# Kernel optimization log

Measured on AMD Instinct MI355X. Metric: run time of the kernel, lower is better.

The kernel has to match this reference:

```python
import jax, jax.numpy as jnp
import numpy as np

B = 4          # documents per batch
L = 128        # unique candidate entity links
S = 2048       # predicted spans (max over batch)
N = 1 + L + S  # root + links + spans


def setup_inputs() -> dict:
    key = jax.random.key(0)
    k1, k2, k3 = jax.random.split(key, 3)
    # coref/linking edge scores over [root | links | spans] x [root | links | spans]
    scores = jax.random.normal(k1, (B, N, N), dtype=jnp.float32) * 0.1
    eye = jnp.eye(N, dtype=jnp.float32)
    # z mask: all admissible edges -- no self loops, no incoming edges to root
    z_mask = jnp.ones((B, N, N), dtype=jnp.float32) * (1.0 - eye)[None]
    z_mask = z_mask.at[:, :, 0].set(0.0)
    # target mask: sparse subset of z edges + root->all so a spanning
    # arborescence always exists (mirrors the gold cluster / gold link edges)
    tgt = (jax.random.uniform(k2, (B, N, N)) < 0.05).astype(jnp.float32) * z_mask
    tgt = tgt.at[:, 0, 1:].set(1.0)
    # ragged valid lengths per batch element (1 + unique_links_len + n_pred_spans)
    lengths = jnp.array([N, N - 256, N - 512, N - 64], dtype=jnp.int32)
    return {"scores": scores, "target_mask": tgt, "z_mask": z_mask, "lengths": lengths}


def _mtt_log_partition(scores, mask, lengths):
    """Matrix-tree theorem log-partition: logdet of the root-minor of the
    Laplacian of exp(scores) restricted to edges in `mask` and to the first
    `lengths[b]` nodes of each batch element."""
    n = scores.shape[-1]
    valid = (jnp.arange(n)[None, :] < lengths[:, None]).astype(scores.dtype)  # [B,N]
    w = jnp.exp(scores) * mask * valid[:, :, None] * valid[:, None, :]        # [B,N,N]
    colsum = jnp.sum(w, axis=-2)                                              # incoming weight per node
    lap = colsum[:, :, None] * jnp.eye(n, dtype=scores.dtype)[None] - w       # L = D_in - W
    minor = lap[:, 1:, 1:]                                                    # drop root row/col
    # pad the diagonal of invalid (past-length) nodes with 1 so they
    # contribute logdet 0 instead of making the minor singular
    pad = 1.0 - valid[:, 1:]
    minor = minor + pad[:, :, None] * jnp.eye(n - 1, dtype=scores.dtype)[None]
    _, logdet = jnp.linalg.slogdet(minor)
    return logdet


def reference(scores, target_mask, z_mask, lengths):
    log_z = _mtt_log_partition(scores, z_mask, lengths)        # log partition over all arborescences
    log_t = _mtt_log_partition(scores, target_mask, lengths)   # log weight of gold arborescences
    return jnp.mean(log_z - log_t)                             # MTT negative log-likelihood
```

## Files before the change

### kernel.cpp

```cpp
#include <hip/hip_runtime.h>
#include <math.h>

#define NFULL 2177
#define NN    2176
#define NB    64
#define NMAT  8
#define NBATCH 4


__global__ void init_cs_kernel(float* __restrict__ cs) {
  int i = blockIdx.x * blockDim.x + threadIdx.x;
  if (i < NMAT * NN) cs[i] = 0.f;
}

__global__ void colsum_kernel(const float* __restrict__ scores,
                              const float* __restrict__ zm,
                              const float* __restrict__ tm,
                              const int* __restrict__ lengths,
                              float* __restrict__ cs) {
  int c = blockIdx.x * blockDim.x + threadIdx.x;
  if (c >= NN) return;
  int rc = blockIdx.y;
  int b  = blockIdx.z;
  int len = lengths[b];
  int j = c + 1;
  if (j >= len) return;
  int i0 = rc * 128;
  int i1 = i0 + 128; if (i1 > len) i1 = len;
  if (i0 >= i1) return;
  size_t base = (size_t)b * NFULL * NFULL + j;
  float az = 0.f, at = 0.f;
  for (int i = i0; i < i1; ++i) {
    size_t off = base + (size_t)i * NFULL;
    float e = __expf(scores[off]);
    az += e * zm[off];
    at += e * tm[off];
  }
  atomicAdd(&cs[b * NN + c], az);
  atomicAdd(&cs[(NBATCH + b) * NN + c], at);
}

__global__ void build_kernel(const float* __restrict__ scores,
                             const float* __restrict__ zm,
                             const float* __restrict__ tm,
                             const int* __restrict__ lengths,
                             const float* __restrict__ cs,
                             float* __restrict__ M) {
  int c = blockIdx.x * blockDim.x + threadIdx.x;
  if (c >= NN) return;
  int r = blockIdx.y;
  int b = blockIdx.z;
  int len = lengths[b];
  int i = r + 1, j = c + 1;
  float vz = 0.f, vt = 0.f;
  if (i < len && j < len) {
    size_t off = (size_t)b * NFULL * NFULL + (size_t)i * NFULL + j;
    float e = __expf(scores[off]);
    vz = e * zm[off];
    vt = e * tm[off];
  }
  float dz = 0.f, dt = 0.f;
  if (r == c) {
    float pad = (j < len) ? 0.f : 1.f;
    dz = cs[b * NN + c] + pad;
    dt = cs[(NBATCH + b) * NN + c] + pad;
  }
  size_t mo = (size_t)r * NN + c;
  M[(size_t)b * NN * NN + mo]            = dz - vz;
  M[(size_t)(NBATCH + b) * NN * NN + mo] = dt - vt;
}


__global__ __launch_bounds__(256) void factor_diag(float* __restrict__ Mb, int k0) {
  __shared__ float T[64][65];
  int m = blockIdx.x;
  float* A = Mb + (size_t)m * NN * NN;
  int tid = threadIdx.x;
  for (int idx = tid; idx < 64 * 64; idx += 256) {
    int r = idx >> 6, c = idx & 63;
    T[r][c] = A[(size_t)(k0 + r) * NN + (k0 + c)];
  }
  __syncthreads();
  for (int j = 0; j < 63; ++j) {
    float inv = 1.0f / T[j][j];
    for (int r = j + 1 + tid; r < 64; r += 256) T[r][j] *= inv;
    __syncthreads();
    int rem = 63 - j;
    for (int idx = tid; idx < rem * rem; idx += 256) {
      int rr = j + 1 + idx / rem;
      int cc = j + 1 + idx % rem;
      T[rr][cc] -= T[rr][j] * T[j][cc];
    }
    __syncthreads();
  }
  for (int idx = tid; idx < 64 * 64; idx += 256) {
    int r = idx >> 6, c = idx & 63;
    A[(size_t)(k0 + r) * NN + (k0 + c)] = T[r][c];
  }
}

__global__ __launch_bounds__(64) void panel_solve(float* __restrict__ Mb, int k0) {
  __shared__ float D[64][65];
  __shared__ float T[64][65];
  int m    = blockIdx.y;
  int role = blockIdx.z;
  float* A = Mb + (size_t)m * NN * NN;
  int tid = threadIdx.x;
  int obase = k0 + 64 + blockIdx.x * 64;
  for (int idx = tid; idx < 64 * 64; idx += 64) {
    int r = idx >> 6, c = idx & 63;
    D[r][c] = A[(size_t)(k0 + r) * NN + (k0 + c)];
  }
  if (role == 0) {
    for (int idx = tid; idx < 64 * 64; idx += 64) {
      int r = idx >> 6, c = idx & 63;
      T[r][c] = A[(size_t)(obase + r) * NN + (k0 + c)];
    }
    __syncthreads();
    for (int j = 0; j < 64; ++j) {
      float acc = T[tid][j];
      for (int t = 0; t < j; ++t) acc -= T[tid][t] * D[t][j];
      T[tid][j] = acc / D[j][j];
    }
    __syncthreads();
    for (int idx = tid; idx < 64 * 64; idx += 64) {
      int r = idx >> 6, c = idx & 63;
      A[(size_t)(obase + r) * NN + (k0 + c)] = T[r][c];
    }
  } else {
    for (int idx = tid; idx < 64 * 64; idx += 64) {
      int r = idx >> 6, c = idx & 63;
      T[r][c] = A[(size_t)(k0 + r) * NN + (obase + c)];
    }
    __syncthreads();
    int c = tid;
    for (int j = 1; j < 64; ++j) {
      float acc = T[j][c];
      for (int t = 0; t < j; ++t) acc -= D[j][t] * T[t][c];
      T[j][c] = acc;
    }
    __syncthreads();
    for (int idx = tid; idx < 64 * 64; idx += 64) {
      int r = idx >> 6, c = idx & 63;
      A[(size_t)(k0 + r) * NN + (obase + c)] = T[r][c];
    }
  }
}

__global__ __launch_bounds__(256) void trail_gemm(float* __restrict__ Mb, int k0) {
  __shared__ float Lt[64][68];
  __shared__ float Ut[64][68];
  int m = blockIdx.z;
  float* A = Mb + (size_t)m * NN * NN;
  int base  = k0 + 64;
  int rbase = base + blockIdx.y * 64;
  int cbase = base + blockIdx.x * 64;
  int tid = threadIdx.x;
  for (int idx = tid; idx < 64 * 64; idx += 256) {
    int r = idx >> 6, k = idx & 63;
    Lt[k][r] = A[(size_t)(rbase + r) * NN + (k0 + k)];
  }
  for (int idx = tid; idx < 64 * 64; idx += 256) {
    int k = idx >> 6, c = idx & 63;
    Ut[k][c] = A[(size_t)(k0 + k) * NN + (cbase + c)];
  }
  __syncthreads();
  int c0 = (tid & 15) << 2;
  int r0 = (tid >> 4) << 2;
  float acc[4][4];
#pragma unroll
  for (int i = 0; i < 4; ++i)
#pragma unroll
    for (int jj = 0; jj < 4; ++jj) acc[i][jj] = 0.f;
#pragma unroll 8
  for (int k = 0; k < 64; ++k) {
    float4 a  = *(const float4*)&Lt[k][r0];
    float4 bv = *(const float4*)&Ut[k][c0];
    acc[0][0] += a.x * bv.x; acc[0][1] += a.x * bv.y; acc[0][2] += a.x * bv.z; acc[0][3] += a.x * bv.w;
    acc[1][0] += a.y * bv.x; acc[1][1] += a.y * bv.y; acc[1][2] += a.y * bv.z; acc[1][3] += a.y * bv.w;
    acc[2][0] += a.z * bv.x; acc[2][1] += a.z * bv.y; acc[2][2] += a.z * bv.z; acc[2][3] += a.z * bv.w;
    acc[3][0] += a.w * bv.x; acc[3][1] += a.w * bv.y; acc[3][2] += a.w * bv.z; acc[3][3] += a.w * bv.w;
  }
#pragma unroll
  for (int i = 0; i < 4; ++i) {
    float4* p = (float4*)&A[(size_t)(rbase + r0 + i) * NN + (cbase + c0)];
    float4 v = *p;
    v.x -= acc[i][0]; v.y -= acc[i][1]; v.z -= acc[i][2]; v.w -= acc[i][3];
    *p = v;
  }
}


__global__ void logdet_kernel(const float* __restrict__ Mb, double* __restrict__ dlog) {
  int m = blockIdx.x;
  const float* A = Mb + (size_t)m * NN * NN;
  double s = 0.0;
  for (int i = threadIdx.x; i < NN; i += 256)
    s += (double)logf(fabsf(A[(size_t)i * NN + i]));
  __shared__ double red[256];
  red[threadIdx.x] = s;
  __syncthreads();
  for (int k = 128; k > 0; k >>= 1) {
    if (threadIdx.x < k) red[threadIdx.x] += red[threadIdx.x + k];
    __syncthreads();
  }
  if (threadIdx.x == 0) dlog[m] = red[0];
}

__global__ void final_kernel(const double* __restrict__ dlog, float* __restrict__ out) {
  if (threadIdx.x == 0) {
    double acc = 0.0;
    for (int b = 0; b < NBATCH; ++b) acc += dlog[b] - dlog[NBATCH + b];
    out[0] = (float)(acc * 0.25);
  }
}


extern "C" void kernel_launch(void* const* d_in, const int* in_sizes, int n_in,
                              void* d_out, int out_size, void* d_ws, size_t ws_size,
                              hipStream_t stream) {
  const float* scores  = (const float*)d_in[0];
  const float* tm      = (const float*)d_in[1];
  const float* zm      = (const float*)d_in[2];
  const int*   lengths = (const int*)d_in[3];
  float* out = (float*)d_out;

  float* M  = (float*)d_ws;
  float* cs = M + (size_t)NMAT * NN * NN;
  double* dlog = (double*)(cs + (size_t)NMAT * NN);

  init_cs_kernel<<<(NMAT * NN + 255) / 256, 256, 0, stream>>>(cs);
  colsum_kernel<<<dim3((NN + 255) / 256, (NFULL + 127) / 128, NBATCH), 256, 0, stream>>>(
      scores, zm, tm, lengths, cs);
  build_kernel<<<dim3((NN + 255) / 256, NN, NBATCH), 256, 0, stream>>>(
      scores, zm, tm, lengths, cs, M);

  for (int k0 = 0; k0 < NN; k0 += NB) {
    factor_diag<<<NMAT, 256, 0, stream>>>(M, k0);
    int rem = NN - k0 - NB;
    if (rem > 0) {
      panel_solve<<<dim3(rem / 64, NMAT, 2), 64, 0, stream>>>(M, k0);
      trail_gemm<<<dim3(rem / 64, rem / 64, NMAT), 256, 0, stream>>>(M, k0);
    }
  }

  logdet_kernel<<<NMAT, 256, 0, stream>>>(M, dlog);
  final_kernel<<<1, 64, 0, stream>>>(dlog, out);
}
```

Before: 4.548 ms.

## Replace triangular panel solves with inverse-block GEMMs and fuse diag factor into trailing update

The 64x64 diagonal block is factored inside the trailing-update kernel by the (0,0) tile block, which also forms explicit inverses of its U and unit-L factors. The panel triangular solves then become 64x64 GEMMs run by 256-thread blocks, replacing the serial per-thread substitution loops in 64-thread blocks. The separate factor_diag launch per step goes away, and the colsum and build kernels are fused into one pass with a small diagonal-fix kernel. The aim is to cut serial panel-solve latency and launch count in the roughly 34-step loop. The cost is some numerical risk from explicit triangular inverses, and serialized work in one block of the trailing kernel.

```diff
diff --git a/kernel.cpp b/kernel.cpp
--- a/kernel.cpp
+++ b/kernel.cpp
@@ -13,74 +13,66 @@
   if (i < NMAT * NN) cs[i] = 0.f;
 }
 
-__global__ void colsum_kernel(const float* __restrict__ scores,
-                              const float* __restrict__ zm,
-                              const float* __restrict__ tm,
-                              const int* __restrict__ lengths,
-                              float* __restrict__ cs) {
-  int c = blockIdx.x * blockDim.x + threadIdx.x;
+__global__ __launch_bounds__(256) void build_fused(const float* __restrict__ scores,
+                                                   const float* __restrict__ zm,
+                                                   const float* __restrict__ tm,
+                                                   const int* __restrict__ lengths,
+                                                   float* __restrict__ cs,
+                                                   float* __restrict__ M) {
+  int c = blockIdx.x * 256 + threadIdx.x;
   if (c >= NN) return;
-  int rc = blockIdx.y;
-  int b  = blockIdx.z;
+  int b = blockIdx.z;
   int len = lengths[b];
   int j = c + 1;
-  if (j >= len) return;
-  int i0 = rc * 128;
-  int i1 = i0 + 128; if (i1 > len) i1 = len;
-  if (i0 >= i1) return;
-  size_t base = (size_t)b * NFULL * NFULL + j;
+  bool jv = (j < len);
+  int r0 = blockIdx.y * 64;
+  size_t sbase = (size_t)b * NFULL * NFULL + j;
   float az = 0.f, at = 0.f;
-  for (int i = i0; i < i1; ++i) {
-    size_t off = base + (size_t)i * NFULL;
-    float e = __expf(scores[off]);
-    az += e * zm[off];
-    at += e * tm[off];
-  }
-  atomicAdd(&cs[b * NN + c], az);
-  atomicAdd(&cs[(NBATCH + b) * NN + c], at);
-}
-
-__global__ void build_kernel(const float* __restrict__ scores,
-                             const float* __restrict__ zm,
-                             const float* __restrict__ tm,
-                             const int* __restrict__ lengths,
-                             const float* __restrict__ cs,
-                             float* __restrict__ M) {
-  int c = blockIdx.x * blockDim.x + threadIdx.x;
-  if (c >= NN) return;
-  int r = blockIdx.y;
-  int b = blockIdx.z;
-  int len = lengths[b];
-  int i = r + 1, j = c + 1;
-  float vz = 0.f, vt = 0.f;
-  if (i < len && j < len) {
-    size_t off = (size_t)b * NFULL * NFULL + (size_t)i * NFULL + j;
-    float e = __expf(scores[off]);
-    vz = e * zm[off];
-    vt = e * tm[off];
-  }
-  float dz = 0.f, dt = 0.f;
-  if (r == c) {
-    float pad = (j < len) ? 0.f : 1.f;
-    dz = cs[b * NN + c] + pad;
-    dt = cs[(NBATCH + b) * NN + c] + pad;
-  }
-  size_t mo = (size_t)r * NN + c;
-  M[(size_t)b * NN * NN + mo]            = dz - vz;
-  M[(size_t)(NBATCH + b) * NN * NN + mo] = dt - vt;
-}
-
-
-__global__ __launch_bounds__(256) void factor_diag(float* __restrict__ Mb, int k0) {
-  __shared__ float T[64][65];
-  int m = blockIdx.x;
-  float* A = Mb + (size_t)m * NN * NN;
-  int tid = threadIdx.x;
-  for (int idx = tid; idx < 64 * 64; idx += 256) {
-    int r = idx >> 6, c = idx & 63;
-    T[r][c] = A[(size_t)(k0 + r) * NN + (k0 + c)];
-  }
-  __syncthreads();
+  if (blockIdx.y == 0 && jv) {
+    float e = __expf(scores[sbase]);
+    az += e * zm[sbase];
+    at += e * tm[sbase];
+  }
+  size_t mz = (size_t)b * NN * NN + (size_t)r0 * NN + c;
+  size_t mt = (size_t)(NBATCH + b) * NN * NN + (size_t)r0 * NN + c;
+  for (int rr = 0; rr < 64; ++rr) {
+    int i = r0 + rr + 1;
+    float vz = 0.f, vt = 0.f;
+    if (jv && i < len) {
+      size_t off = sbase + (size_t)i * NFULL;
+      float e = __expf(scores[off]);
+      vz = e * zm[off];
+      vt = e * tm[off];
+      az += vz;
+      at += vt;
+    }
+    M[mz] = -vz;
+    M[mt] = -vt;
+    mz += NN;
+    mt += NN;
+  }
+  if (az != 0.f) atomicAdd(&cs[b * NN + c], az);
+  if (at != 0.f) atomicAdd(&cs[(NBATCH + b) * NN + c], at);
+}
+
+__global__ void diag_fix(const int* __restrict__ lengths,
+                         const float* __restrict__ cs,
+                         float* __restrict__ M) {
+  int idx = blockIdx.x * 256 + threadIdx.x;
+  if (idx >= NMAT * NN) return;
+  int mm = idx / NN, c = idx - mm * NN;
+  int len = lengths[mm & 3];
+  float pad = (c + 1 < len) ? 0.f : 1.f;
+  M[(size_t)mm * NN * NN + (size_t)c * NN + c] = cs[idx] + pad;
+}
+
+
+__device__ void factor_invert(float* __restrict__ A,
+                              float* __restrict__ invUg,
+                              float* __restrict__ invLg,
+                              float (*T)[68], float (*X)[68],
+                              float* __restrict__ Dinv,
+                              int k0, int tid, int do_inv) {
   for (int j = 0; j < 63; ++j) {
     float inv = 1.0f / T[j][j];
     for (int r = j + 1 + tid; r < 64; r += 256) T[r][j] *= inv;
@@ -97,59 +89,120 @@
     int r = idx >> 6, c = idx & 63;
     A[(size_t)(k0 + r) * NN + (k0 + c)] = T[r][c];
   }
-}
-
-__global__ __launch_bounds__(64) void panel_solve(float* __restrict__ Mb, int k0) {
-  __shared__ float D[64][65];
-  __shared__ float T[64][65];
-  int m    = blockIdx.y;
-  int role = blockIdx.z;
+  if (!do_inv) return;
+  if (tid < 64) Dinv[tid] = 1.0f / T[tid][tid];
+  __syncthreads();
+  if (tid < 64) {
+    int j = tid;
+    X[j][j] = Dinv[j];
+    for (int i = j - 1; i >= 0; --i) {
+      float s = 0.f;
+      for (int t = i + 1; t <= j; ++t) s += T[i][t] * X[t][j];
+      X[i][j] = -s * Dinv[i];
+    }
+    for (int i = j + 1; i < 64; ++i) X[i][j] = 0.f;
+  }
+  __syncthreads();
+  for (int idx = tid; idx < 4096; idx += 256) invUg[idx] = X[idx >> 6][idx & 63];
+  __syncthreads();
+  if (tid < 64) {
+    int j = tid;
+    X[j][j] = 1.f;
+    for (int i = j + 1; i < 64; ++i) {
+      float s = 0.f;
+      for (int t = j; t < i; ++t) s += T[i][t] * X[t][j];
+      X[i][j] = -s;
+    }
+    for (int i = 0; i < j; ++i) X[i][j] = 0.f;
+  }
+  __syncthreads();
+  for (int idx = tid; idx < 4096; idx += 256) invLg[idx] = X[idx >> 6][idx & 63];
+}
+
+__global__ __launch_bounds__(256) void factor0(float* __restrict__ Mb,
+                                               float* __restrict__ invUb,
+                                               float* __restrict__ invLb) {
+  __shared__ float T[64][68];
+  __shared__ float X[64][68];
+  __shared__ float Dinv[64];
+  int m = blockIdx.x, tid = threadIdx.x;
   float* A = Mb + (size_t)m * NN * NN;
-  int tid = threadIdx.x;
+  for (int idx = tid; idx < 64 * 64; idx += 256) {
+    int r = idx >> 6, c = idx & 63;
+    T[r][c] = A[(size_t)r * NN + c];
+  }
+  __syncthreads();
+  factor_invert(A, invUb + (size_t)m * 4096, invLb + (size_t)m * 4096,
+                T, X, Dinv, 0, tid, 1);
+}
+
+__global__ __launch_bounds__(256) void panel_gemm(float* __restrict__ Mb,
+                                                  const float* __restrict__ invUb,
+                                                  const float* __restrict__ invLb,
+                                                  int k0) {
+  __shared__ float Aa[64][68];
+  __shared__ float Bb[64][68];
+  int m = blockIdx.y, role = blockIdx.z, tid = threadIdx.x;
+  float* A = Mb + (size_t)m * NN * NN;
   int obase = k0 + 64 + blockIdx.x * 64;
-  for (int idx = tid; idx < 64 * 64; idx += 64) {
-    int r = idx >> 6, c = idx & 63;
-    D[r][c] = A[(size_t)(k0 + r) * NN + (k0 + c)];
-  }
   if (role == 0) {
-    for (int idx = tid; idx < 64 * 64; idx += 64) {
-      int r = idx >> 6, c = idx & 63;
-      T[r][c] = A[(size_t)(obase + r) * NN + (k0 + c)];
-    }
-    __syncthreads();
-    for (int j = 0; j < 64; ++j) {
-      float acc = T[tid][j];
-      for (int t = 0; t < j; ++t) acc -= T[tid][t] * D[t][j];
-      T[tid][j] = acc / D[j][j];
-    }
-    __syncthreads();
-    for (int idx = tid; idx < 64 * 64; idx += 64) {
-      int r = idx >> 6, c = idx & 63;
-      A[(size_t)(obase + r) * NN + (k0 + c)] = T[r][c];
-    }
+    const float* invU = invUb + (size_t)m * 4096;
+    for (int idx = tid; idx < 4096; idx += 256) {
+      int r = idx >> 6, k = idx & 63;
+      Aa[k][r] = A[(size_t)(obase + r) * NN + (k0 + k)];
+    }
+    for (int idx = tid; idx < 4096; idx += 256)
+      Bb[idx >> 6][idx & 63] = invU[idx];
   } else {
-    for (int idx = tid; idx < 64 * 64; idx += 64) {
-      int r = idx >> 6, c = idx & 63;
-      T[r][c] = A[(size_t)(k0 + r) * NN + (obase + c)];
-    }
-    __syncthreads();
-    int c = tid;
-    for (int j = 1; j < 64; ++j) {
-      float acc = T[j][c];
-      for (int t = 0; t < j; ++t) acc -= D[j][t] * T[t][c];
-      T[j][c] = acc;
-    }
-    __syncthreads();
-    for (int idx = tid; idx < 64 * 64; idx += 64) {
-      int r = idx >> 6, c = idx & 63;
-      A[(size_t)(k0 + r) * NN + (obase + c)] = T[r][c];
-    }
-  }
-}
-
-__global__ __launch_bounds__(256) void trail_gemm(float* __restrict__ Mb, int k0) {
+    const float* invL = invLb + (size_t)m * 4096;
+    for (int idx = tid; idx < 4096; idx += 256) {
+      int r = idx >> 6, k = idx & 63;
+      Aa[k][r] = invL[(r << 6) + k];
+    }
+    for (int idx = tid; idx < 4096; idx += 256) {
+      int k = idx >> 6, c = idx & 63;
+      Bb[k][c] = A[(size_t)(k0 + k) * NN + (obase + c)];
+    }
+  }
+  __syncthreads();
+  int c0 = (tid & 15) << 2;
+  int r0 = (tid >> 4) << 2;
+  float acc[4][4];
+#pragma unroll
+  for (int i = 0; i < 4; ++i)
+#pragma unroll
+    for (int jj = 0; jj < 4; ++jj) acc[i][jj] = 0.f;
+#pragma unroll 8
+  for (int k = 0; k < 64; ++k) {
+    float4 a  = *(const float4*)&Aa[k][r0];
+    float4 bv = *(const float4*)&Bb[k][c0];
+    acc[0][0] += a.x * bv.x; acc[0][1] += a.x * bv.y; acc[0][2] += a.x * bv.z; acc[0][3] += a.x * bv.w;
+    acc[1][0] += a.y * bv.x; acc[1][1] += a.y * bv.y; acc[1][2] += a.y * bv.z; acc[1][3] += a.y * bv.w;
+    acc[2][0] += a.z * bv.x; acc[2][1] += a.z * bv.y; acc[2][2] += a.z * bv.z; acc[2][3] += a.z * bv.w;
+    acc[3][0] += a.w * bv.x; acc[3][1] += a.w * bv.y; acc[3][2] += a.w * bv.z; acc[3][3] += a.w * bv.w;
+  }
+  if (role == 0) {
+#pragma unroll
+    for (int i = 0; i < 4; ++i) {
+      float4 v = make_float4(acc[i][0], acc[i][1], acc[i][2], acc[i][3]);
+      *(float4*)&A[(size_t)(obase + r0 + i) * NN + (k0 + c0)] = v;
+    }
+  } else {
+#pragma unroll
+    for (int i = 0; i < 4; ++i) {
+      float4 v = make_float4(acc[i][0], acc[i][1], acc[i][2], acc[i][3]);
+      *(float4*)&A[(size_t)(k0 + r0 + i) * NN + (obase + c0)] = v;
+    }
+  }
+}
+
+__global__ __launch_bounds__(256) void trail_gemm(float* __restrict__ Mb,
+                                                  float* __restrict__ invUb,
+                                                  float* __restrict__ invLb,
+                                                  int k0, int do_inv) {
   __shared__ float Lt[64][68];
   __shared__ float Ut[64][68];
+  __shared__ float Dinv[64];
   int m = blockIdx.z;
   float* A = Mb + (size_t)m * NN * NN;
   int base  = k0 + 64;
@@ -181,13 +234,28 @@
     acc[2][0] += a.z * bv.x; acc[2][1] += a.z * bv.y; acc[2][2] += a.z * bv.z; acc[2][3] += a.z * bv.w;
     acc[3][0] += a.w * bv.x; acc[3][1] += a.w * bv.y; acc[3][2] += a.w * bv.z; acc[3][3] += a.w * bv.w;
   }
+  bool special = (blockIdx.x == 0 && blockIdx.y == 0);
+  if (!special) {
+#pragma unroll
+    for (int i = 0; i < 4; ++i) {
+      float4* p = (float4*)&A[(size_t)(rbase + r0 + i) * NN + (cbase + c0)];
+      float4 v = *p;
+      v.x -= acc[i][0]; v.y -= acc[i][1]; v.z -= acc[i][2]; v.w -= acc[i][3];
+      *p = v;
+    }
+    return;
+  }
+  __syncthreads();
 #pragma unroll
   for (int i = 0; i < 4; ++i) {
-    float4* p = (float4*)&A[(size_t)(rbase + r0 + i) * NN + (cbase + c0)];
+    const float4* p = (const float4*)&A[(size_t)(rbase + r0 + i) * NN + (cbase + c0)];
     float4 v = *p;
     v.x -= acc[i][0]; v.y -= acc[i][1]; v.z -= acc[i][2]; v.w -= acc[i][3];
-    *p = v;
-  }
+    *(float4*)&Lt[r0 + i][c0] = v;
+  }
+  __syncthreads();
+  factor_invert(A, invUb + (size_t)m * 4096, invLb + (size_t)m * 4096,
+                Lt, Ut, Dinv, base, tid, do_inv);
 }
 
 
@@ -228,20 +296,20 @@
   float* M  = (float*)d_ws;
   float* cs = M + (size_t)NMAT * NN * NN;
   double* dlog = (double*)(cs + (size_t)NMAT * NN);
+  float* invU = (float*)(dlog + NMAT);
+  float* invL = invU + (size_t)NMAT * 4096;
 
   init_cs_kernel<<<(NMAT * NN + 255) / 256, 256, 0, stream>>>(cs);
-  colsum_kernel<<<dim3((NN + 255) / 256, (NFULL + 127) / 128, NBATCH), 256, 0, stream>>>(
-      scores, zm, tm, lengths, cs);
-  build_kernel<<<dim3((NN + 255) / 256, NN, NBATCH), 256, 0, stream>>>(
+  build_fused<<<dim3((NN + 255) / 256, NN / 64, NBATCH), 256, 0, stream>>>(
       scores, zm, tm, lengths, cs, M);
-
-  for (int k0 = 0; k0 < NN; k0 += NB) {
-    factor_diag<<<NMAT, 256, 0, stream>>>(M, k0);
+  diag_fix<<<(NMAT * NN + 255) / 256, 256, 0, stream>>>(lengths, cs, M);
+  factor0<<<NMAT, 256, 0, stream>>>(M, invU, invL);
+
+  for (int k0 = 0; k0 + NB < NN; k0 += NB) {
     int rem = NN - k0 - NB;
-    if (rem > 0) {
-      panel_solve<<<dim3(rem / 64, NMAT, 2), 64, 0, stream>>>(M, k0);
-      trail_gemm<<<dim3(rem / 64, rem / 64, NMAT), 256, 0, stream>>>(M, k0);
-    }
+    panel_gemm<<<dim3(rem / 64, NMAT, 2), 256, 0, stream>>>(M, invU, invL, k0);
+    trail_gemm<<<dim3(rem / 64, rem / 64, NMAT), 256, 0, stream>>>(
+        M, invU, invL, k0, rem > 64 ? 1 : 0);
   }
 
   logdet_kernel<<<NMAT, 256, 0, stream>>>(M, dlog);
```

Result: slower. 5.321 ms (+17.0%).
